# Performance work log

Measured on AMD Instinct MI355X. Metric: run time of the kernel, lower is better.

## Reference

```python
import math
import jax, jax.numpy as jnp
import numpy as np

B, N, H, NH, DD, L = 4, 384, 256, 8, 32, 4
HD = H // NH
V = 11           # num_species + 1 (padding row 0)
CUTOFF = 5.0

def _ln(x, g, b):
    m = jnp.mean(x, axis=-1, keepdims=True)
    v = jnp.mean(jnp.square(x - m), axis=-1, keepdims=True)
    return (x - m) / jnp.sqrt(v + 1e-5) * g + b

def setup_inputs() -> dict:
    key = jax.random.key(0)
    ks = iter(jax.random.split(key, 64))
    def nrm(shape, s=0.05):
        return jax.random.normal(next(ks), shape, jnp.float32) * s
    return {
        'node_indices': jax.random.randint(next(ks), (B, N), 0, V),
        'positions': jax.random.normal(next(ks), (B, N, 3), jnp.float32),
        'mask': jnp.ones((B, N), jnp.float32),
        'emb': nrm((V, H)).at[0].set(0.0),
        'ln1_g': jnp.ones((L, H)), 'ln1_b': jnp.zeros((L, H)),
        'qkv_w': nrm((L, H, 3 * H)), 'qkv_b': jnp.zeros((L, 3 * H)),
        'out_w': nrm((L, H, H)), 'out_b': jnp.zeros((L, H)),
        'rb_w1': nrm((L, DD, H)), 'rb_b1': jnp.zeros((L, H)),
        'rb_w2': nrm((L, H, NH)), 'rb_b2': jnp.zeros((L, NH)),
        'gate_w1': nrm((L, H, H)), 'gate_b1': jnp.zeros((L, H)),
        'gate_w2': nrm((L, H, H)), 'gate_b2': jnp.zeros((L, H)),
        'ln2_g': jnp.ones((L, H)), 'ln2_b': jnp.zeros((L, H)),
        'ff_w1': nrm((L, H, 2 * H)), 'ff_b1': jnp.zeros((L, 2 * H)),
        'ff_w2': nrm((L, 2 * H, H)), 'ff_b2': jnp.zeros((L, H)),
        'pool_g': jnp.ones((H,)), 'pool_beta': jnp.zeros((H,)),
        'pool_w': nrm((H, H)), 'pool_b': jnp.zeros((H,)),
        'eh_w': nrm((H, 1)), 'eh_b': jnp.zeros((1,)),
    }

def _forward(node_indices, positions, mask, emb, ln1_g, ln1_b, qkv_w, qkv_b,
             out_w, out_b, rb_w1, rb_b1, rb_w2, rb_b2, gate_w1, gate_b1,
             gate_w2, gate_b2, ln2_g, ln2_b, ff_w1, ff_b1, ff_w2, ff_b2,
             pool_g, pool_beta, pool_w, pool_b, eh_w, eh_b):
    mask_b = mask > 0
    x = emb[node_indices] * mask_b[..., None]               # [B,N,H]
    pos = positions * mask_b[..., None].astype(positions.dtype)
    rel = pos[:, :, None, :] - pos[:, None, :, :]           # [B,N,N,3]
    dist = jnp.linalg.norm(rel + 1e-9, axis=-1)             # [B,N,N]
    adj = (dist <= CUTOFF).astype(jnp.float32)
    adj = adj * mask_b[:, None, :] * mask_b[:, :, None]
    edge = adj > 0
    isolated = mask_b & ~edge.any(axis=-1)
    adj = adj + isolated.astype(jnp.float32)[:, :, None] * jnp.eye(N, dtype=jnp.float32)
    edge = adj > 0
    # Bessel envelope features [B,N,N,DD]
    kk = jnp.arange(1, DD + 1, dtype=jnp.float32)
    ang = math.pi * kk * (dist / CUTOFF)[..., None]
    feat = jnp.sin(ang) / (dist[..., None] + 1e-6)
    feat = feat * (dist <= CUTOFF)[..., None].astype(jnp.float32)
    feat = feat * adj[..., None]

    scale = math.sqrt(HD)
    NEG = jnp.finfo(jnp.float32).min
    for l in range(L):
        res = x
        h = _ln(x, ln1_g[l], ln1_b[l])
        qkv = h @ qkv_w[l] + qkv_b[l]
        q, k, v = jnp.split(qkv, 3, axis=-1)
        q = q.reshape(B, N, NH, HD)
        k = k.reshape(B, N, NH, HD)
        v = v.reshape(B, N, NH, HD)
        logits = jnp.einsum('bihd,bjhd->bhij', q, k) / scale
        hb = jax.nn.silu(feat @ rb_w1[l] + rb_b1[l])        # [B,N,N,H]
        bias = hb @ rb_w2[l] + rb_b2[l]                     # [B,N,N,NH]
        logits = logits + bias.transpose(0, 3, 1, 2)
        logits = jnp.where(edge[:, None, :, :], logits, NEG)
        attn = jax.nn.softmax(logits, axis=-1)
        ctx = jnp.einsum('bhij,bjhd->bihd', attn, v).reshape(B, N, H)
        gated = jax.nn.silu(h @ gate_w1[l] + gate_b1[l]) @ gate_w2[l] + gate_b2[l]
        x = res + ((ctx * jax.nn.sigmoid(gated)) @ out_w[l] + out_b[l])
        y = _ln(x, ln2_g[l], ln2_b[l])
        x = x + (jax.nn.gelu(y @ ff_w1[l] + ff_b1[l], approximate=False) @ ff_w2[l] + ff_b2[l])

    pooled = jax.nn.silu(_ln(x, pool_g, pool_beta) @ pool_w + pool_b)
    masked = pooled * mask_b[..., None]
    counts = jnp.maximum(jnp.sum(mask_b, axis=1), 1)
    graph = jnp.sum(masked, axis=1) / counts[:, None]
    energy = (graph @ eh_w + eh_b)[:, 0]                    # [B]
    return energy

def reference(node_indices, positions, mask, emb, ln1_g, ln1_b, qkv_w, qkv_b,
              out_w, out_b, rb_w1, rb_b1, rb_w2, rb_b2, gate_w1, gate_b1,
              gate_w2, gate_b2, ln2_g, ln2_b, ff_w1, ff_b1, ff_w2, ff_b2,
              pool_g, pool_beta, pool_w, pool_b, eh_w, eh_b):
    return _forward(node_indices, positions, mask, emb, ln1_g, ln1_b, qkv_w,
                    qkv_b, out_w, out_b, rb_w1, rb_b1, rb_w2, rb_b2, gate_w1,
                    gate_b1, gate_w2, gate_b2, ln2_g, ln2_b, ff_w1, ff_b1,
                    ff_w2, ff_b2, pool_g, pool_beta, pool_w, pool_b, eh_w, eh_b)
```

## Files before the change

### kernel.cpp

```cpp
#include <hip/hip_runtime.h>
#include <hip/hip_bf16.h>
#include <math.h>

constexpr int B_ = 4, N_ = 384, H_ = 256, NH_ = 8, DD_ = 32, L_ = 4;
constexpr int M_ = B_ * N_;
constexpr float CUT = 5.0f;
constexpr float PI_ = 3.14159265358979323846f;
constexpr float INVSC = 0.17677669529663687f;
constexpr int TBL_N = 4096;
constexpr int TBL_STRIDE = 4098;

typedef __attribute__((ext_vector_type(8))) short short8;
typedef __attribute__((ext_vector_type(4))) float f32x4;
typedef __attribute__((ext_vector_type(4))) unsigned short u16x4;
using u16 = unsigned short;

__device__ __forceinline__ u16 f2b(float f) {
  __hip_bfloat16 h = __float2bfloat16(f);
  return *reinterpret_cast<u16*>(&h);
}
__device__ __forceinline__ float b2f(u16 u) {
  __hip_bfloat16 h;
  *reinterpret_cast<u16*>(&h) = u;
  return __bfloat162float(h);
}

__device__ __forceinline__ float wave_sum(float v) {
#pragma unroll
  for (int s = 1; s < 64; s <<= 1) v += __shfl_xor(v, s);
  return v;
}

__global__ __launch_bounds__(256) void embed_k(const int* __restrict__ idx,
                                               const float* __restrict__ mask,
                                               const float* __restrict__ emb,
                                               float* __restrict__ X) {
  int e = blockIdx.x * 256 + threadIdx.x;
  int mrow = e >> 8, c = e & 255;
  float mb = mask[mrow] > 0.f ? 1.f : 0.f;
  X[e] = emb[idx[mrow] * H_ + c] * mb;
}

__global__ __launch_bounds__(256) void table_k(const float* __restrict__ rb_w1,
                                               const float* __restrict__ rb_b1,
                                               const float* __restrict__ rb_w2,
                                               const float* __restrict__ rb_b2,
                                               float* __restrict__ tbl2) {
  constexpr int TT = 64;
  int l = blockIdx.y;
  int t0 = blockIdx.x * TT;
  int tid = threadIdx.x;
  __shared__ float sfA[TT][32];
  __shared__ float hbA[TT][260];
#pragma unroll
  for (int m = 0; m < 8; m++) {
    int idx = m * 256 + tid;
    int tl = idx >> 5, k = idx & 31;
    int t = t0 + tl;
    float d = (t <= TBL_N) ? (t * (CUT / (float)TBL_N)) : 1.7320508075688772e-9f;
    float ang = PI_ * (k + 1) * d * (1.f / CUT);
    sfA[tl][k] = sinf(ang) / (d + 1e-6f);
  }
  __syncthreads();
  float w1c[32];
  const float* w1 = rb_w1 + (size_t)l * DD_ * H_;
#pragma unroll
  for (int k = 0; k < 32; k++) w1c[k] = w1[k * H_ + tid];
  float b1v = rb_b1[l * H_ + tid];
  for (int tl = 0; tl < TT; tl++) {
    float pre = b1v;
    const float4* sfp = (const float4*)sfA[tl];
#pragma unroll
    for (int kq = 0; kq < 8; kq++) {
      float4 s4 = sfp[kq];
      pre += s4.x * w1c[kq * 4] + s4.y * w1c[kq * 4 + 1] + s4.z * w1c[kq * 4 + 2] +
             s4.w * w1c[kq * 4 + 3];
    }
    hbA[tl][tid] = pre / (1.f + __expf(-pre));
  }
  __syncthreads();
  const float* w2 = rb_w2 + (size_t)l * H_ * NH_;
  int o = tid & 7;
  float b2v = rb_b2[l * NH_ + o];
#pragma unroll
  for (int half = 0; half < 2; half++) {
    int tl = (tid >> 3) + half * 32;
    float acc = b2v;
    const float4* hp = (const float4*)hbA[tl];
#pragma unroll 4
    for (int hq = 0; hq < 64; hq++) {
      float4 h4 = hp[hq];
      acc += h4.x * w2[(hq * 4 + 0) * NH_ + o] + h4.y * w2[(hq * 4 + 1) * NH_ + o] +
             h4.z * w2[(hq * 4 + 2) * NH_ + o] + h4.w * w2[(hq * 4 + 3) * NH_ + o];
    }
    int t = t0 + tl;
    if (t <= TBL_STRIDE) tbl2[(size_t)t * 32 + l * NH_ + o] = acc;
  }
}

__global__ __launch_bounds__(256) void bias_all2_k(const float* __restrict__ pos,
                                                   const float* __restrict__ mask,
                                                   const float* __restrict__ tbl2,
                                                   u16* __restrict__ biasb) {
  int e = blockIdx.x * 256 + threadIdx.x;
  int j = e % N_;
  int t = e / N_;
  int i = t % N_;
  int b = t / N_;
  float mi = mask[b * N_ + i], mj = mask[b * N_ + j];
  const float* pi = pos + (size_t)(b * N_ + i) * 3;
  const float* pj = pos + (size_t)(b * N_ + j) * 3;
  float dx = pi[0] - pj[0] + 1e-9f;
  float dy = pi[1] - pj[1] + 1e-9f;
  float dz = pi[2] - pj[2] + 1e-9f;
  float d = sqrtf(dx * dx + dy * dy + dz * dz);
  bool edge = (mi > 0.f && mj > 0.f) && (d <= CUT);
  size_t plane = (size_t)N_ * N_;
  size_t obase = (size_t)b * NH_ * plane + (size_t)i * N_ + j;
  size_t lstride = (size_t)B_ * NH_ * plane;
  if (edge) {
    int ixrow;
    float fr;
    if (i == j) {
      ixrow = TBL_N + 1;
      fr = 0.f;
    } else {
      float u = d * ((float)TBL_N / CUT);
      int ix = (int)u;
      ix = ix > TBL_N - 1 ? TBL_N - 1 : ix;
      fr = u - (float)ix;
      ixrow = ix;
    }
    const float4* r0 = (const float4*)(tbl2 + (size_t)ixrow * 32);
    const float4* r1 = (const float4*)(tbl2 + (size_t)(ixrow + 1) * 32);
    float4 a0[8], a1[8];
#pragma unroll
    for (int q = 0; q < 8; q++) {
      a0[q] = r0[q];
      a1[q] = r1[q];
    }
    float w0 = 1.f - fr;
#pragma unroll
    for (int q = 0; q < 8; q++) {
      float v0[4] = {a0[q].x, a0[q].y, a0[q].z, a0[q].w};
      float v1[4] = {a1[q].x, a1[q].y, a1[q].z, a1[q].w};
#pragma unroll
      for (int c = 0; c < 4; c++) {
        int lh = q * 4 + c;
        int l = lh >> 3, h = lh & 7;
        float v = v0[c] * w0 + v1[c] * fr;
        biasb[(size_t)l * lstride + obase + (size_t)h * plane] = f2b(v);
      }
    }
  } else {
#pragma unroll
    for (int lh = 0; lh < 32; lh++) {
      int l = lh >> 3, h = lh & 7;
      biasb[(size_t)l * lstride + obase + (size_t)h * plane] = 0xFF80;
    }
  }
}

__global__ __launch_bounds__(256) void ln_k(const float* __restrict__ X,
                                            const float* __restrict__ g,
                                            const float* __restrict__ bta,
                                            u16* __restrict__ O) {
  int wave = threadIdx.x >> 6, lane = threadIdx.x & 63;
  int row = blockIdx.x * 4 + wave;
  const float* xr = X + (size_t)row * H_;
  float4 v = *(const float4*)(xr + lane * 4);
  float s = v.x + v.y + v.z + v.w;
  s = wave_sum(s);
  float m = s * (1.f / H_);
  float dx = v.x - m, dy = v.y - m, dz = v.z - m, dw = v.w - m;
  float vs = dx * dx + dy * dy + dz * dz + dw * dw;
  vs = wave_sum(vs);
  float rs = rsqrtf(vs * (1.f / H_) + 1e-5f);
  float4 gg = *(const float4*)(g + lane * 4);
  float4 bb = *(const float4*)(bta + lane * 4);
  u16x4 o;
  o[0] = f2b(dx * rs * gg.x + bb.x);
  o[1] = f2b(dy * rs * gg.y + bb.y);
  o[2] = f2b(dz * rs * gg.z + bb.z);
  o[3] = f2b(dw * rs * gg.w + bb.w);
  *(u16x4*)(O + (size_t)row * H_ + lane * 4) = o;
}

struct TrJob {
  const float* src;
  u16* dst;
  int K, N, nx, ny, nz, base, dstride;
};
struct TrJobs {
  TrJob j[7];
};
__global__ __launch_bounds__(256) void tr_all_k(TrJobs jobs) {
  __shared__ float t[32][33];
  int bid = blockIdx.x;
  int ji = 0;
#pragma unroll
  for (int q = 1; q < 7; q++)
    if (bid >= jobs.j[q].base) ji = q;
  const TrJob& J = jobs.j[ji];
  int local = bid - J.base;
  int z = local / (J.nx * J.ny);
  int r2 = local % (J.nx * J.ny);
  int ky = r2 / J.nx, kx = r2 % J.nx;
  int n0 = kx * 32, k0 = ky * 32;
  const float* s = J.src + (size_t)z * J.K * J.N;
  u16* d = J.dst + (size_t)z * J.dstride;
  int tid = threadIdx.x;
  int r = tid >> 3, c4 = (tid & 7) * 4;
  float4 v = *(const float4*)(s + (size_t)(k0 + r) * J.N + n0 + c4);
  t[r][c4 + 0] = v.x;
  t[r][c4 + 1] = v.y;
  t[r][c4 + 2] = v.z;
  t[r][c4 + 3] = v.w;
  __syncthreads();
  u16x4 o;
  o[0] = f2b(t[c4 + 0][r]);
  o[1] = f2b(t[c4 + 1][r]);
  o[2] = f2b(t[c4 + 2][r]);
  o[3] = f2b(t[c4 + 3][r]);
  *(u16x4*)(d + (size_t)(n0 + r) * J.K + k0 + c4) = o;
}

template <int ACT, bool RES, bool PRE, bool OBF>
__device__ __forceinline__ void mgemm_body(u16* __restrict__ As, u16* __restrict__ Bs,
                                           const void* __restrict__ Av,
                                           const u16* __restrict__ WT,
                                           const float* __restrict__ bias,
                                           const float* __restrict__ resid,
                                           void* __restrict__ Cv, int K, int Nc,
                                           int lda, const float* __restrict__ G,
                                           const float* __restrict__ bias2,
                                           int m0, int n0) {
  const int tid = threadIdx.x;
  const int wave = tid >> 6, lane = tid & 63;
  const int wr = wave >> 1, wc = wave & 1, lr = lane & 15, lg = lane >> 4;
  f32x4 acc[2][2] = {};
  const int srow = tid >> 2, sp = tid & 3;
  for (int k0 = 0; k0 < K; k0 += 128) {
#pragma unroll
    for (int s4 = 0; s4 < 4; s4++) {
      int s = sp * 4 + s4;
      int phys = s ^ (srow & 15);
      if (PRE) {
        const float* ap = (const float*)Av + (size_t)(m0 + srow) * lda + k0 + s * 8;
        const float* gp = G + (size_t)(m0 + srow) * lda + k0 + s * 8;
        float4 a0 = *(const float4*)ap;
        float4 a1 = *(const float4*)(ap + 4);
        float4 g0 = *(const float4*)gp;
        float4 g1 = *(const float4*)(gp + 4);
        short8 vv;
        vv[0] = (short)f2b(a0.x / (1.f + __expf(-g0.x)));
        vv[1] = (short)f2b(a0.y / (1.f + __expf(-g0.y)));
        vv[2] = (short)f2b(a0.z / (1.f + __expf(-g0.z)));
        vv[3] = (short)f2b(a0.w / (1.f + __expf(-g0.w)));
        vv[4] = (short)f2b(a1.x / (1.f + __expf(-g1.x)));
        vv[5] = (short)f2b(a1.y / (1.f + __expf(-g1.y)));
        vv[6] = (short)f2b(a1.z / (1.f + __expf(-g1.z)));
        vv[7] = (short)f2b(a1.w / (1.f + __expf(-g1.w)));
        *(short8*)&As[srow * 128 + phys * 8] = vv;
      } else {
        const u16* Ab = (const u16*)Av;
        short8 v = *(const short8*)(Ab + (size_t)(m0 + srow) * lda + k0 + s * 8);
        *(short8*)&As[srow * 128 + phys * 8] = v;
      }
      short8 w = *(const short8*)(WT + (size_t)(n0 + srow) * K + k0 + s * 8);
      *(short8*)&Bs[srow * 128 + phys * 8] = w;
    }
    __syncthreads();
#pragma unroll
    for (int kk = 0; kk < 4; kk++) {
      int slot = kk * 4 + lg;
      short8 af[2], bf_[2];
#pragma unroll
      for (int i = 0; i < 2; i++) {
        int row = wr * 32 + i * 16 + lr;
        af[i] = *(const short8*)&As[row * 128 + (slot ^ (row & 15)) * 8];
      }
#pragma unroll
      for (int j = 0; j < 2; j++) {
        int row = wc * 32 + j * 16 + lr;
        bf_[j] = *(const short8*)&Bs[row * 128 + (slot ^ (row & 15)) * 8];
      }
#pragma unroll
      for (int i = 0; i < 2; i++)
#pragma unroll
        for (int j = 0; j < 2; j++)
          acc[i][j] = __builtin_amdgcn_mfma_f32_16x16x32_bf16(af[i], bf_[j], acc[i][j], 0, 0, 0);
    }
    __syncthreads();
  }
#pragma unroll
  for (int i = 0; i < 2; i++)
#pragma unroll
    for (int j = 0; j < 2; j++)
#pragma unroll
      for (int rg = 0; rg < 4; rg++) {
        int row = m0 + wr * 32 + i * 16 + lg * 4 + rg;
        int col = n0 + wc * 32 + j * 16 + lr;
        float v;
        if (ACT == 3) {
          float bv = (col < 768) ? bias[col] : bias2[col - 768];
          v = acc[i][j][rg] + bv;
          if (col >= 768) v = v / (1.f + __expf(-v));
        } else {
          v = acc[i][j][rg] + bias[col];
          if (ACT == 1) v = v / (1.f + __expf(-v));
          if (ACT == 2) v = 0.5f * v * (1.f + erff(v * 0.70710678118654752f));
        }
        if (RES) v += resid[(size_t)row * Nc + col];
        if (OBF)
          ((u16*)Cv)[(size_t)row * Nc + col] = f2b(v);
        else
          ((float*)Cv)[(size_t)row * Nc + col] = v;
      }
}

template <int ACT, bool RES, bool PRE, bool OBF>
__global__ __launch_bounds__(256) void mgemm_k(const void* __restrict__ Av,
                                               const u16* __restrict__ WT,
                                               const float* __restrict__ bias,
                                               const float* __restrict__ resid,
                                               void* __restrict__ Cv, int K, int Nc,
                                               int lda, const float* __restrict__ G,
                                               const float* __restrict__ bias2) {
  __shared__ u16 As[64 * 128];
  __shared__ u16 Bs[64 * 128];
  mgemm_body<ACT, RES, PRE, OBF>(As, Bs, Av, WT, bias, resid, Cv, K, Nc, lda, G, bias2,
                                 blockIdx.y * 64, blockIdx.x * 64);
}

__device__ __forceinline__ void attn_body(u16* __restrict__ FragQ, u16* __restrict__ FragK,
                                          u16* __restrict__ FragV, float* __restrict__ smax,
                                          float* __restrict__ ssum,
                                          const u16* __restrict__ qkv,
                                          const u16* __restrict__ biasb,
                                          float* __restrict__ ctx, int qs,
                                          int it, int hh, int b) {
  u16* FragP = FragK;
  float* pbuf = (float*)FragV;
  const int i0 = it * 32;
  const int tid = threadIdx.x;
  const size_t bb = (size_t)b * N_;

  if (tid < 128) {
    int q = tid >> 2, dc = tid & 3;
    short8 v = *(const short8*)(qkv + (bb + i0 + q) * qs + hh * 32 + dc * 8);
    *(short8*)&FragQ[(((q >> 4) * 64) + (q & 15) + 16 * dc) * 8] = v;
  }
#pragma unroll
  for (int m = 0; m < 6; m++) {
    int idx = m * 256 + tid;
    int key = idx >> 2, dc = idx & 3;
    const u16* kb = qkv + (bb + key) * qs + 256 + hh * 32 + dc * 8;
    short8 kv = *(const short8*)kb;
    *(short8*)&FragK[(((key >> 4) * 64) + (key & 15) + 16 * dc) * 8] = kv;
    short8 vv = *(const short8*)(kb + 256);
    int kc = key >> 5, sub = (key >> 3) & 3, kj = key & 7;
#pragma unroll
    for (int j = 0; j < 8; j++) {
      int d = dc * 8 + j;
      FragV[(((kc * 2 + (d >> 4)) * 64) + (d & 15) + 16 * sub) * 8 + kj] = (u16)vv[j];
    }
  }
  __syncthreads();

  const int wave = tid >> 6, lane = tid & 63;
  const int rh = wave & 1, kh = wave >> 1;
  const int g = lane >> 4, c = lane & 15;
  const u16* bptr = biasb + (size_t)(b * NH_ + hh) * N_ * N_;

  short8 qf = *(const short8*)&FragQ[(rh * 64 + lane) * 8];
  f32x4 sc[12];
#pragma unroll
  for (int t = 0; t < 12; t++) {
    int T = kh * 12 + t;
    short8 kf = *(const short8*)&FragK[(T * 64 + lane) * 8];
    f32x4 z = {0.f, 0.f, 0.f, 0.f};
    sc[t] = __builtin_amdgcn_mfma_f32_16x16x32_bf16(qf, kf, z, 0, 0, 0);
    int key = 16 * T + c;
#pragma unroll
    for (int reg = 0; reg < 4; reg++) {
      int row = i0 + 16 * rh + 4 * g + reg;
      float bv = b2f(bptr[(size_t)row * N_ + key]);
      sc[t][reg] = sc[t][reg] * INVSC + bv;
    }
  }
  float mx[4];
#pragma unroll
  for (int reg = 0; reg < 4; reg++) {
    float m = sc[0][reg];
#pragma unroll
    for (int t = 1; t < 12; t++) m = fmaxf(m, sc[t][reg]);
#pragma unroll
    for (int s = 1; s < 16; s <<= 1) m = fmaxf(m, __shfl_xor(m, s));
    mx[reg] = m;
  }
  if (c == 0) {
#pragma unroll
    for (int reg = 0; reg < 4; reg++) smax[kh * 32 + 16 * rh + 4 * g + reg] = mx[reg];
  }
  __syncthreads();
  float sm[4];
#pragma unroll
  for (int reg = 0; reg < 4; reg++) {
    float M = fmaxf(smax[16 * rh + 4 * g + reg], smax[32 + 16 * rh + 4 * g + reg]);
    float s = 0.f;
#pragma unroll
    for (int t = 0; t < 12; t++) {
      float p = __expf(sc[t][reg] - M);
      sc[t][reg] = p;
      s += p;
    }
    sm[reg] = s;
  }
#pragma unroll
  for (int reg = 0; reg < 4; reg++) {
#pragma unroll
    for (int s = 1; s < 16; s <<= 1) sm[reg] += __shfl_xor(sm[reg], s);
  }
  if (c == 0) {
#pragma unroll
    for (int reg = 0; reg < 4; reg++) ssum[kh * 32 + 16 * rh + 4 * g + reg] = sm[reg];
  }
#pragma unroll
  for (int t = 0; t < 12; t++) {
    int T = kh * 12 + t;
    int kc = T >> 1;
    int sub = (2 * T + (c >> 3)) & 3;
#pragma unroll
    for (int reg = 0; reg < 4; reg++) {
      FragP[((rh * 12 + kc) * 64 + (4 * g + reg) + 16 * sub) * 8 + (c & 7)] =
          f2b(sc[t][reg]);
    }
  }
  __syncthreads();
  float Ls[4];
#pragma unroll
  for (int reg = 0; reg < 4; reg++)
    Ls[reg] = ssum[16 * rh + 4 * g + reg] + ssum[32 + 16 * rh + 4 * g + reg];

  f32x4 pcc[2] = {};
#pragma unroll
  for (int t = 0; t < 6; t++) {
    int kc = kh * 6 + t;
    short8 pf = *(const short8*)&FragP[((rh * 12 + kc) * 64 + lane) * 8];
#pragma unroll
    for (int nh = 0; nh < 2; nh++) {
      short8 vf = *(const short8*)&FragV[((kc * 2 + nh) * 64 + lane) * 8];
      pcc[nh] = __builtin_amdgcn_mfma_f32_16x16x32_bf16(pf, vf, pcc[nh], 0, 0, 0);
    }
  }
  __syncthreads();
  if (kh == 1) {
#pragma unroll
    for (int nh = 0; nh < 2; nh++)
#pragma unroll
      for (int reg = 0; reg < 4; reg++)
        pbuf[rh * 512 + (4 * g + reg) * 32 + nh * 16 + c] = pcc[nh][reg];
  }
  __syncthreads();
  if (kh == 0) {
#pragma unroll
    for (int nh = 0; nh < 2; nh++)
#pragma unroll
      for (int reg = 0; reg < 4; reg++) {
        float v = pcc[nh][reg] + pbuf[rh * 512 + (4 * g + reg) * 32 + nh * 16 + c];
        int row = i0 + 16 * rh + 4 * g + reg;
        ctx[(bb + row) * H_ + hh * 32 + nh * 16 + c] = v / Ls[reg];
      }
  }
}

__global__ __launch_bounds__(256) void attn_g2_k(const u16* __restrict__ qkv,
                                                 const u16* __restrict__ biasb,
                                                 float* __restrict__ ctx,
                                                 const u16* __restrict__ wg2,
                                                 const float* __restrict__ gb2,
                                                 float* __restrict__ g2) {
  __shared__ __align__(16) u16 SMEM[(2 + 24 + 24) * 64 * 8];
  __shared__ float sred[2 * 32 * 2];
  int bid = blockIdx.x;
  if (bid < 384) {
    int it = bid % 12;
    int t = bid / 12;
    attn_body(SMEM, SMEM + 1024, SMEM + 1024 + 12288, sred, sred + 64,
              qkv, biasb, ctx, 1024, it, t % NH_, t / NH_);
  } else {
    int g = bid - 384;
    mgemm_body<0, false, false, false>(SMEM, SMEM + 8192, (const void*)(qkv + 768), wg2,
                                       gb2, nullptr, g2, 256, 256, 1024, nullptr,
                                       nullptr, (g >> 2) * 64, (g & 3) * 64);
  }
}

__global__ __launch_bounds__(256) void energy_k(const float* __restrict__ p2,
                                                const float* __restrict__ mask,
                                                const float* __restrict__ ehw,
                                                const float* __restrict__ ehb,
                                                float* __restrict__ out) {
  int b = blockIdx.x, h = threadIdx.x;
  float s = 0.f, cnt = 0.f;
#pragma unroll 4
  for (int i = 0; i < N_; i++) {
    float m = mask[b * N_ + i] > 0.f ? 1.f : 0.f;
    s += p2[(size_t)(b * N_ + i) * H_ + h] * m;
    cnt += m;
  }
  float val = s * ehw[h];
  __shared__ float red[256];
  red[h] = val;
  __syncthreads();
  for (int st = 128; st > 0; st >>= 1) {
    if (h < st) red[h] += red[h + st];
    __syncthreads();
  }
  if (h == 0) {
    float c = cnt < 1.f ? 1.f : cnt;
    out[b] = red[0] / c + ehb[0];
  }
}

extern "C" void kernel_launch(void* const* d_in, const int* in_sizes, int n_in,
                              void* d_out, int out_size, void* d_ws, size_t ws_size,
                              hipStream_t stream) {
  const int* node_idx = (const int*)d_in[0];
  const float* positions = (const float*)d_in[1];
  const float* mask = (const float*)d_in[2];
  const float* emb = (const float*)d_in[3];
  const float* ln1_g = (const float*)d_in[4];
  const float* ln1_b = (const float*)d_in[5];
  const float* qkv_w = (const float*)d_in[6];
  const float* qkv_b = (const float*)d_in[7];
  const float* out_w = (const float*)d_in[8];
  const float* out_b = (const float*)d_in[9];
  const float* rb_w1 = (const float*)d_in[10];
  const float* rb_b1 = (const float*)d_in[11];
  const float* rb_w2 = (const float*)d_in[12];
  const float* rb_b2 = (const float*)d_in[13];
  const float* gate_w1 = (const float*)d_in[14];
  const float* gate_b1 = (const float*)d_in[15];
  const float* gate_w2 = (const float*)d_in[16];
  const float* gate_b2 = (const float*)d_in[17];
  const float* ln2_g = (const float*)d_in[18];
  const float* ln2_b = (const float*)d_in[19];
  const float* ff_w1 = (const float*)d_in[20];
  const float* ff_b1 = (const float*)d_in[21];
  const float* ff_w2 = (const float*)d_in[22];
  const float* ff_b2 = (const float*)d_in[23];
  const float* pool_g = (const float*)d_in[24];
  const float* pool_beta = (const float*)d_in[25];
  const float* pool_w = (const float*)d_in[26];
  const float* pool_b = (const float*)d_in[27];
  const float* eh_w = (const float*)d_in[28];
  const float* eh_b = (const float*)d_in[29];
  float* eout = (float*)d_out;

  char* W8 = (char*)d_ws;
  float* x = (float*)(W8 + 0);
  u16* qgb = (u16*)(W8 + 1572864);
  float* ctx = (float*)(W8 + 4718592);
  float* g2 = (float*)(W8 + 6291456);
  u16* hb = (u16*)(W8 + 7864320);
  u16* ffb = (u16*)(W8 + 8650752);
  float* tbl2 = (float*)(W8 + 12582912);
  u16* wt = (u16*)(W8 + 13631488);
  u16* wt_qg = wt;
  u16* wt_out = wt + 1048576;
  u16* wt_g2 = wt + 1310720;
  u16* wt_f1 = wt + 1572864;
  u16* wt_f2 = wt + 2097152;
  u16* wt_p = wt + 2621440;
  u16* biasb = (u16*)(W8 + 19005440);
  const size_t bias_lstride = (size_t)B_ * NH_ * N_ * N_;

  embed_k<<<M_ * H_ / 256, 256, 0, stream>>>(node_idx, mask, emb, x);
  table_k<<<dim3(65, L_), 256, 0, stream>>>(rb_w1, rb_b1, rb_w2, rb_b2, tbl2);
  {
    TrJobs jobs;
    jobs.j[0] = {qkv_w, wt_qg, 256, 768, 24, 8, 4, 0, 262144};
    jobs.j[1] = {gate_w1, wt_qg + 768 * 256, 256, 256, 8, 8, 4, 768, 262144};
    jobs.j[2] = {out_w, wt_out, 256, 256, 8, 8, 4, 1024, 65536};
    jobs.j[3] = {gate_w2, wt_g2, 256, 256, 8, 8, 4, 1280, 65536};
    jobs.j[4] = {ff_w1, wt_f1, 256, 512, 16, 8, 4, 1536, 131072};
    jobs.j[5] = {ff_w2, wt_f2, 512, 256, 8, 16, 4, 2048, 131072};
    jobs.j[6] = {pool_w, wt_p, 256, 256, 8, 8, 1, 2560, 65536};
    tr_all_k<<<2624, 256, 0, stream>>>(jobs);
  }
  bias_all2_k<<<B_ * N_ * N_ / 256, 256, 0, stream>>>(positions, mask, tbl2, biasb);

  for (int l = 0; l < L_; l++) {
    const float* qb = qkv_b + (size_t)l * 3 * H_;
    const float* ob = out_b + (size_t)l * H_;
    const float* gb1 = gate_b1 + (size_t)l * H_;
    const float* gb2 = gate_b2 + (size_t)l * H_;
    const float* fb1 = ff_b1 + (size_t)l * 2 * H_;
    const float* fb2 = ff_b2 + (size_t)l * H_;
    u16* wqg = wt_qg + (size_t)l * 1024 * 256;
    u16* wo = wt_out + (size_t)l * 256 * 256;
    u16* wg2 = wt_g2 + (size_t)l * 256 * 256;
    u16* wf1 = wt_f1 + (size_t)l * 512 * 256;
    u16* wf2 = wt_f2 + (size_t)l * 256 * 512;

    ln_k<<<M_ / 4, 256, 0, stream>>>(x, ln1_g + l * H_, ln1_b + l * H_, hb);
    mgemm_k<3, false, false, true><<<dim3(16, 24), 256, 0, stream>>>(
        hb, wqg, qb, nullptr, qgb, 256, 1024, 256, nullptr, gb1);
    attn_g2_k<<<480, 256, 0, stream>>>(qgb, biasb + (size_t)l * bias_lstride, ctx,
                                       wg2, gb2, g2);
    mgemm_k<0, true, true, false><<<dim3(4, 24), 256, 0, stream>>>(
        ctx, wo, ob, x, x, 256, 256, 256, g2, nullptr);
    ln_k<<<M_ / 4, 256, 0, stream>>>(x, ln2_g + l * H_, ln2_b + l * H_, hb);
    mgemm_k<2, false, false, true><<<dim3(8, 24), 256, 0, stream>>>(
        hb, wf1, fb1, nullptr, ffb, 256, 512, 256, nullptr, nullptr);
    mgemm_k<0, true, false, false><<<dim3(4, 24), 256, 0, stream>>>(
        ffb, wf2, fb2, x, x, 512, 256, 512, nullptr, nullptr);
  }

  ln_k<<<M_ / 4, 256, 0, stream>>>(x, pool_g, pool_beta, hb);
  mgemm_k<1, false, false, false><<<dim3(4, 24), 256, 0, stream>>>(
      hb, wt_p, pool_b, nullptr, ctx, 256, 256, 256, nullptr, nullptr);
  energy_k<<<B_, 256, 0, stream>>>(ctx, mask, eh_w, eh_b, eout);
}
```

Before: 289.0 us.

## Merge setup kernels into one launch and co-schedule bias build with first QKV GEMM

Folds the embedding, radial-basis table and weight-transpose kernels into a single block-indexed setup kernel. The pairwise bias construction moves into the layer-0 QKV GEMM launch as extra blocks, so the two independent jobs share one grid and can overlap. This removes several launches and the gaps between them. In exchange, the setup kernel reserves the largest shared-memory footprint of all its branches, which may lower occupancy for the small transpose and embed blocks, and bias blocks now compete with GEMM blocks for compute units.

```diff
diff --git a/kernel.cpp b/kernel.cpp
--- a/kernel.cpp
+++ b/kernel.cpp
@@ -31,78 +31,11 @@
   return v;
 }
 
-__global__ __launch_bounds__(256) void embed_k(const int* __restrict__ idx,
-                                               const float* __restrict__ mask,
-                                               const float* __restrict__ emb,
-                                               float* __restrict__ X) {
-  int e = blockIdx.x * 256 + threadIdx.x;
-  int mrow = e >> 8, c = e & 255;
-  float mb = mask[mrow] > 0.f ? 1.f : 0.f;
-  X[e] = emb[idx[mrow] * H_ + c] * mb;
-}
-
-__global__ __launch_bounds__(256) void table_k(const float* __restrict__ rb_w1,
-                                               const float* __restrict__ rb_b1,
-                                               const float* __restrict__ rb_w2,
-                                               const float* __restrict__ rb_b2,
-                                               float* __restrict__ tbl2) {
-  constexpr int TT = 64;
-  int l = blockIdx.y;
-  int t0 = blockIdx.x * TT;
-  int tid = threadIdx.x;
-  __shared__ float sfA[TT][32];
-  __shared__ float hbA[TT][260];
-#pragma unroll
-  for (int m = 0; m < 8; m++) {
-    int idx = m * 256 + tid;
-    int tl = idx >> 5, k = idx & 31;
-    int t = t0 + tl;
-    float d = (t <= TBL_N) ? (t * (CUT / (float)TBL_N)) : 1.7320508075688772e-9f;
-    float ang = PI_ * (k + 1) * d * (1.f / CUT);
-    sfA[tl][k] = sinf(ang) / (d + 1e-6f);
-  }
-  __syncthreads();
-  float w1c[32];
-  const float* w1 = rb_w1 + (size_t)l * DD_ * H_;
-#pragma unroll
-  for (int k = 0; k < 32; k++) w1c[k] = w1[k * H_ + tid];
-  float b1v = rb_b1[l * H_ + tid];
-  for (int tl = 0; tl < TT; tl++) {
-    float pre = b1v;
-    const float4* sfp = (const float4*)sfA[tl];
-#pragma unroll
-    for (int kq = 0; kq < 8; kq++) {
-      float4 s4 = sfp[kq];
-      pre += s4.x * w1c[kq * 4] + s4.y * w1c[kq * 4 + 1] + s4.z * w1c[kq * 4 + 2] +
-             s4.w * w1c[kq * 4 + 3];
-    }
-    hbA[tl][tid] = pre / (1.f + __expf(-pre));
-  }
-  __syncthreads();
-  const float* w2 = rb_w2 + (size_t)l * H_ * NH_;
-  int o = tid & 7;
-  float b2v = rb_b2[l * NH_ + o];
-#pragma unroll
-  for (int half = 0; half < 2; half++) {
-    int tl = (tid >> 3) + half * 32;
-    float acc = b2v;
-    const float4* hp = (const float4*)hbA[tl];
-#pragma unroll 4
-    for (int hq = 0; hq < 64; hq++) {
-      float4 h4 = hp[hq];
-      acc += h4.x * w2[(hq * 4 + 0) * NH_ + o] + h4.y * w2[(hq * 4 + 1) * NH_ + o] +
-             h4.z * w2[(hq * 4 + 2) * NH_ + o] + h4.w * w2[(hq * 4 + 3) * NH_ + o];
-    }
-    int t = t0 + tl;
-    if (t <= TBL_STRIDE) tbl2[(size_t)t * 32 + l * NH_ + o] = acc;
-  }
-}
-
-__global__ __launch_bounds__(256) void bias_all2_k(const float* __restrict__ pos,
-                                                   const float* __restrict__ mask,
-                                                   const float* __restrict__ tbl2,
-                                                   u16* __restrict__ biasb) {
-  int e = blockIdx.x * 256 + threadIdx.x;
+
+__device__ __forceinline__ void bias_item(const float* __restrict__ pos,
+                                          const float* __restrict__ mask,
+                                          const float* __restrict__ tbl2,
+                                          u16* __restrict__ biasb, int e) {
   int j = e % N_;
   int t = e / N_;
   int i = t % N_;
@@ -161,6 +94,112 @@
   }
 }
 
+struct TrJob {
+  const float* src;
+  u16* dst;
+  int K, N, nx, ny, nz, base, dstride;
+};
+struct TrJobs {
+  TrJob j[7];
+};
+__global__ __launch_bounds__(256) void setup_all_k(TrJobs jobs,
+                                                   const float* __restrict__ rb_w1,
+                                                   const float* __restrict__ rb_b1,
+                                                   const float* __restrict__ rb_w2,
+                                                   const float* __restrict__ rb_b2,
+                                                   float* __restrict__ tbl2,
+                                                   const int* __restrict__ nidx,
+                                                   const float* __restrict__ mask,
+                                                   const float* __restrict__ emb,
+                                                   float* __restrict__ X) {
+  __shared__ float sfA[64][32];
+  __shared__ float hbA[64][260];
+  __shared__ float t[32][33];
+  int bid = blockIdx.x;
+  int tid = threadIdx.x;
+  if (bid < 260) {
+    constexpr int TT = 64;
+    int l = bid / 65;
+    int t0 = (bid % 65) * TT;
+#pragma unroll
+    for (int m = 0; m < 8; m++) {
+      int idx = m * 256 + tid;
+      int tl = idx >> 5, k = idx & 31;
+      int tt = t0 + tl;
+      float d = (tt <= TBL_N) ? (tt * (CUT / (float)TBL_N)) : 1.7320508075688772e-9f;
+      float ang = PI_ * (k + 1) * d * (1.f / CUT);
+      sfA[tl][k] = sinf(ang) / (d + 1e-6f);
+    }
+    __syncthreads();
+    float w1c[32];
+    const float* w1 = rb_w1 + (size_t)l * DD_ * H_;
+#pragma unroll
+    for (int k = 0; k < 32; k++) w1c[k] = w1[k * H_ + tid];
+    float b1v = rb_b1[l * H_ + tid];
+    for (int tl = 0; tl < TT; tl++) {
+      float pre = b1v;
+      const float4* sfp = (const float4*)sfA[tl];
+#pragma unroll
+      for (int kq = 0; kq < 8; kq++) {
+        float4 s4 = sfp[kq];
+        pre += s4.x * w1c[kq * 4] + s4.y * w1c[kq * 4 + 1] + s4.z * w1c[kq * 4 + 2] +
+               s4.w * w1c[kq * 4 + 3];
+      }
+      hbA[tl][tid] = pre / (1.f + __expf(-pre));
+    }
+    __syncthreads();
+    const float* w2 = rb_w2 + (size_t)l * H_ * NH_;
+    int o = tid & 7;
+    float b2v = rb_b2[l * NH_ + o];
+#pragma unroll
+    for (int half = 0; half < 2; half++) {
+      int tl = (tid >> 3) + half * 32;
+      float acc = b2v;
+      const float4* hp = (const float4*)hbA[tl];
+#pragma unroll 4
+      for (int hq = 0; hq < 64; hq++) {
+        float4 h4 = hp[hq];
+        acc += h4.x * w2[(hq * 4 + 0) * NH_ + o] + h4.y * w2[(hq * 4 + 1) * NH_ + o] +
+               h4.z * w2[(hq * 4 + 2) * NH_ + o] + h4.w * w2[(hq * 4 + 3) * NH_ + o];
+      }
+      int tt = t0 + tl;
+      if (tt <= TBL_STRIDE) tbl2[(size_t)tt * 32 + l * NH_ + o] = acc;
+    }
+  } else if (bid < 2884) {
+    int tb = bid - 260;
+    int ji = 0;
+#pragma unroll
+    for (int q = 1; q < 7; q++)
+      if (tb >= jobs.j[q].base) ji = q;
+    const TrJob& J = jobs.j[ji];
+    int local = tb - J.base;
+    int z = local / (J.nx * J.ny);
+    int r2 = local % (J.nx * J.ny);
+    int ky = r2 / J.nx, kx = r2 % J.nx;
+    int n0 = kx * 32, k0 = ky * 32;
+    const float* s = J.src + (size_t)z * J.K * J.N;
+    u16* d = J.dst + (size_t)z * J.dstride;
+    int r = tid >> 3, c4 = (tid & 7) * 4;
+    float4 v = *(const float4*)(s + (size_t)(k0 + r) * J.N + n0 + c4);
+    t[r][c4 + 0] = v.x;
+    t[r][c4 + 1] = v.y;
+    t[r][c4 + 2] = v.z;
+    t[r][c4 + 3] = v.w;
+    __syncthreads();
+    u16x4 o;
+    o[0] = f2b(t[c4 + 0][r]);
+    o[1] = f2b(t[c4 + 1][r]);
+    o[2] = f2b(t[c4 + 2][r]);
+    o[3] = f2b(t[c4 + 3][r]);
+    *(u16x4*)(d + (size_t)(n0 + r) * J.K + k0 + c4) = o;
+  } else {
+    int e = (bid - 2884) * 256 + tid;
+    int mrow = e >> 8, c = e & 255;
+    float mb = mask[mrow] > 0.f ? 1.f : 0.f;
+    X[e] = emb[nidx[mrow] * H_ + c] * mb;
+  }
+}
+
 __global__ __launch_bounds__(256) void ln_k(const float* __restrict__ X,
                                             const float* __restrict__ g,
                                             const float* __restrict__ bta,
@@ -184,45 +223,6 @@
   o[2] = f2b(dz * rs * gg.z + bb.z);
   o[3] = f2b(dw * rs * gg.w + bb.w);
   *(u16x4*)(O + (size_t)row * H_ + lane * 4) = o;
-}
-
-struct TrJob {
-  const float* src;
-  u16* dst;
-  int K, N, nx, ny, nz, base, dstride;
-};
-struct TrJobs {
-  TrJob j[7];
-};
-__global__ __launch_bounds__(256) void tr_all_k(TrJobs jobs) {
-  __shared__ float t[32][33];
-  int bid = blockIdx.x;
-  int ji = 0;
-#pragma unroll
-  for (int q = 1; q < 7; q++)
-    if (bid >= jobs.j[q].base) ji = q;
-  const TrJob& J = jobs.j[ji];
-  int local = bid - J.base;
-  int z = local / (J.nx * J.ny);
-  int r2 = local % (J.nx * J.ny);
-  int ky = r2 / J.nx, kx = r2 % J.nx;
-  int n0 = kx * 32, k0 = ky * 32;
-  const float* s = J.src + (size_t)z * J.K * J.N;
-  u16* d = J.dst + (size_t)z * J.dstride;
-  int tid = threadIdx.x;
-  int r = tid >> 3, c4 = (tid & 7) * 4;
-  float4 v = *(const float4*)(s + (size_t)(k0 + r) * J.N + n0 + c4);
-  t[r][c4 + 0] = v.x;
-  t[r][c4 + 1] = v.y;
-  t[r][c4 + 2] = v.z;
-  t[r][c4 + 3] = v.w;
-  __syncthreads();
-  u16x4 o;
-  o[0] = f2b(t[c4 + 0][r]);
-  o[1] = f2b(t[c4 + 1][r]);
-  o[2] = f2b(t[c4 + 2][r]);
-  o[3] = f2b(t[c4 + 3][r]);
-  *(u16x4*)(d + (size_t)(n0 + r) * J.K + k0 + c4) = o;
 }
 
 template <int ACT, bool RES, bool PRE, bool OBF>
@@ -331,6 +331,26 @@
   __shared__ u16 Bs[64 * 128];
   mgemm_body<ACT, RES, PRE, OBF>(As, Bs, Av, WT, bias, resid, Cv, K, Nc, lda, G, bias2,
                                  blockIdx.y * 64, blockIdx.x * 64);
+}
+
+__global__ __launch_bounds__(256) void qkv_bias_k(const u16* __restrict__ hb,
+                                                  const u16* __restrict__ wqg,
+                                                  const float* __restrict__ qb,
+                                                  const float* __restrict__ gb1,
+                                                  u16* __restrict__ qgb,
+                                                  const float* __restrict__ pos,
+                                                  const float* __restrict__ mask,
+                                                  const float* __restrict__ tbl2,
+                                                  u16* __restrict__ biasb) {
+  __shared__ u16 As[64 * 128];
+  __shared__ u16 Bs[64 * 128];
+  int bid = blockIdx.x;
+  if (bid < 384) {
+    mgemm_body<3, false, false, true>(As, Bs, hb, wqg, qb, nullptr, qgb, 256, 1024, 256,
+                                      nullptr, gb1, (bid >> 4) * 64, (bid & 15) * 64);
+  } else {
+    bias_item(pos, mask, tbl2, biasb, (bid - 384) * 256 + threadIdx.x);
+  }
 }
 
 __device__ __forceinline__ void attn_body(u16* __restrict__ FragQ, u16* __restrict__ FragK,
@@ -577,8 +597,6 @@
   u16* biasb = (u16*)(W8 + 19005440);
   const size_t bias_lstride = (size_t)B_ * NH_ * N_ * N_;
 
-  embed_k<<<M_ * H_ / 256, 256, 0, stream>>>(node_idx, mask, emb, x);
-  table_k<<<dim3(65, L_), 256, 0, stream>>>(rb_w1, rb_b1, rb_w2, rb_b2, tbl2);
   {
     TrJobs jobs;
     jobs.j[0] = {qkv_w, wt_qg, 256, 768, 24, 8, 4, 0, 262144};
@@ -588,9 +606,9 @@
     jobs.j[4] = {ff_w1, wt_f1, 256, 512, 16, 8, 4, 1536, 131072};
     jobs.j[5] = {ff_w2, wt_f2, 512, 256, 8, 16, 4, 2048, 131072};
     jobs.j[6] = {pool_w, wt_p, 256, 256, 8, 8, 1, 2560, 65536};
-    tr_all_k<<<2624, 256, 0, stream>>>(jobs);
-  }
-  bias_all2_k<<<B_ * N_ * N_ / 256, 256, 0, stream>>>(positions, mask, tbl2, biasb);
+    setup_all_k<<<4420, 256, 0, stream>>>(jobs, rb_w1, rb_b1, rb_w2, rb_b2, tbl2,
+                                          node_idx, mask, emb, x);
+  }
 
   for (int l = 0; l < L_; l++) {
     const float* qb = qkv_b + (size_t)l * 3 * H_;
@@ -606,8 +624,13 @@
     u16* wf2 = wt_f2 + (size_t)l * 256 * 512;
 
     ln_k<<<M_ / 4, 256, 0, stream>>>(x, ln1_g + l * H_, ln1_b + l * H_, hb);
-    mgemm_k<3, false, false, true><<<dim3(16, 24), 256, 0, stream>>>(
-        hb, wqg, qb, nullptr, qgb, 256, 1024, 256, nullptr, gb1);
+    if (l == 0) {
+      qkv_bias_k<<<2688, 256, 0, stream>>>(hb, wqg, qb, gb1, qgb, positions, mask, tbl2,
+                                           biasb);
+    } else {
+      mgemm_k<3, false, false, true><<<dim3(16, 24), 256, 0, stream>>>(
+          hb, wqg, qb, nullptr, qgb, 256, 1024, 256, nullptr, gb1);
+    }
     attn_g2_k<<<480, 256, 0, stream>>>(qgb, biasb + (size_t)l * bias_lstride, ctx,
                                        wg2, gb2, g2);
     mgemm_k<0, true, true, false><<<dim3(4, 24), 256, 0, stream>>>(
```

New measurement: 275.9 us. 1.05x faster.
